# Optimization experiments

Hardware: AMD Instinct MI355X
Metric: run time of the kernel (lower is better)

The kernel has to match this reference:

```python
import jax, jax.numpy as jnp
import numpy as np

B, T, C, H, W = 8, 10, 1, 64, 64
HID = 64

def conv2d_same(x, w):
    return jax.lax.conv_general_dilated(x, w, (1, 1), 'SAME', dimension_numbers=('NCHW', 'OIHW', 'NCHW'))

def setup_inputs():
    key = jax.random.key(0)
    ks = iter(jax.random.split(key, 32))
    inp = {'x': jax.random.uniform(next(ks), (B, T, C, H, W), jnp.float32)}
    def cell_params(prefix, in_ch):
        # 4 gates (i, f, g, o) stacked along output channels -> fused gate conv
        inp[prefix + '_Wx'] = jax.random.normal(next(ks), (4 * HID, in_ch, 3, 3), jnp.float32) * 0.05
        inp[prefix + '_Wh'] = jax.random.normal(next(ks), (4 * HID, HID, 3, 3), jnp.float32) * 0.05
        inp[prefix + '_Wc'] = jax.random.normal(next(ks), (4, HID, H, W), jnp.float32) * 0.05
        inp[prefix + '_b'] = jax.random.normal(next(ks), (4, HID, H, W), jnp.float32) * 0.05
    cell_params('enc0', C)
    cell_params('enc1', HID)
    cell_params('dec0', HID)
    cell_params('dec1', HID)
    inp['fin_w'] = jax.random.normal(next(ks), (1, HID, 3, 3), jnp.float32) * 0.05
    inp['fin_b'] = jnp.zeros((1,), jnp.float32)
    inp['prediction_len'] = 10
    return inp

def _cell(Wx, Wh, Wc, b, xt, h, c):
    # gate = act(W_x*x + W_h*h + W_c.c + bias); all 4 gates use the OLD (h, c)
    hid = h.shape[1]
    pre = conv2d_same(xt, Wx) + conv2d_same(h, Wh)  # (B, 4*hid, H, W)
    pre = pre.reshape(pre.shape[0], 4, hid, pre.shape[2], pre.shape[3])
    pre = pre + Wc[None] * c[:, None] + b[None]
    i = jax.nn.sigmoid(pre[:, 0])
    f = jax.nn.sigmoid(pre[:, 1])
    g = jnp.tanh(pre[:, 2])
    o = jax.nn.sigmoid(pre[:, 3])
    c_new = f * c + i * g
    h_new = o * jnp.tanh(c_new)
    return h_new, c_new

def reference(x, enc0_Wx, enc0_Wh, enc0_Wc, enc0_b, enc1_Wx, enc1_Wh, enc1_Wc, enc1_b, dec0_Wx, dec0_Wh, dec0_Wc, dec0_b, dec1_Wx, dec1_Wh, dec1_Wc, dec1_b, fin_w, fin_b, prediction_len):
    b_, t_ = x.shape[0], x.shape[1]
    h_, w_ = x.shape[3], x.shape[4]
    hid = enc0_Wc.shape[1]
    z = jnp.zeros((b_, hid, h_, w_), x.dtype)

    def enc_step(carry, xt):
        h0, c0, h1, c1 = carry
        h0, c0 = _cell(enc0_Wx, enc0_Wh, enc0_Wc, enc0_b, xt, h0, c0)
        h1, c1 = _cell(enc1_Wx, enc1_Wh, enc1_Wc, enc1_b, h0, h1, c1)
        return (h0, c0, h1, c1), None

    (eh0, ec0, eh1, ec1), _ = jax.lax.scan(enc_step, (z, z, z, z), jnp.swapaxes(x, 0, 1))
    state = eh1  # top-layer encoder hidden; decoder h/c start at zeros (as in torch code)

    def dec_step(carry, _):
        s, h0, c0, h1, c1 = carry
        h0, c0 = _cell(dec0_Wx, dec0_Wh, dec0_Wc, dec0_b, s, h0, c0)
        h1, c1 = _cell(dec1_Wx, dec1_Wh, dec1_Wc, dec1_b, h0, h1, c1)
        return (h1, h0, c0, h1, c1), h1

    _, ys = jax.lax.scan(dec_step, (state, z, z, z, z), None, length=prediction_len)
    # ys: (F, B, hid, H, W); Conv3d with (1,3,3) kernel == per-frame 2d conv
    f_ = ys.shape[0]
    y = ys.reshape(f_ * b_, hid, h_, w_)
    y = conv2d_same(y, fin_w) + fin_b[None, :, None, None]
    y = y.reshape(f_, b_, 1, h_, w_)
    return jax.nn.sigmoid(jnp.swapaxes(y, 0, 1))  # (B, F, 1, H, W)
```

## Files before the change

### kernel.cpp

```cpp
#include <hip/hip_runtime.h>
#include <hip/hip_bf16.h>
#include <math.h>

#define BSZ    8
#define TSTEPS 10
#define FLEN   10
#define HID    64
#define HW     4096
#define IMG    (HID * HW)
#define OC4    (4 * HID)
#define PADW   66
#define PPIX   (PADW * PADW)
#define PADIMG (PPIX * HID)
#define PADSZ  (BSZ * PADIMG)
#define SB     (BSZ * IMG)
#define KT_E0  640
#define KT_STD 1152

typedef __attribute__((ext_vector_type(8))) short bf16x8;
typedef __attribute__((ext_vector_type(4))) float f32x4;

__device__ __forceinline__ float sigmoidf_(float x) {
    return 1.0f / (1.0f + __expf(-x));
}
__device__ __forceinline__ float tanh_fast(float x) {
    float e = __expf(2.0f * x);
    return 1.0f - 2.0f / (e + 1.0f);
}
__device__ __forceinline__ float bf2f(short u) {
    union { unsigned u; float f; } cv;
    cv.u = ((unsigned)(unsigned short)u) << 16;
    return cv.f;
}
__device__ __forceinline__ short f2bf(float x) {
    __hip_bfloat16 h = __float2bfloat16(x);
    union { __hip_bfloat16 h; short s; } cv; cv.h = h;
    return cv.s;
}

__global__ __launch_bounds__(256) void reorder_w(
    const float* __restrict__ Wx, int icx,
    const float* __restrict__ Wh, __hip_bfloat16* __restrict__ Bw, int ktot) {
    int ocp = blockIdx.x, hid = ocp >> 2, gate = ocp & 3;
    int oc = gate * 64 + hid;
    for (int k = threadIdx.x; k < ktot; k += 256) {
        int c = k >> 6, j = k & 63;
        float v;
        if (icx == 1) {
            if (c == 0) v = (j < 9) ? Wx[oc * 9 + j] : 0.0f;
            else        v = Wh[(oc * 64 + j) * 9 + (c - 1)];
        } else {
            if (c < 9)  v = Wx[(oc * 64 + j) * 9 + c];
            else        v = Wh[(oc * 64 + j) * 9 + (c - 9)];
        }
        Bw[ocp * ktot + k] = __float2bfloat16(v);
    }
}

__global__ __launch_bounds__(256) void pack_wcb(
    const float* __restrict__ Wc, const float* __restrict__ bias,
    __hip_bfloat16* __restrict__ wcb) {
    int i = blockIdx.x * 256 + threadIdx.x;
    int hid = i >> 12, p = i & 4095;
    union { short s[8]; bf16x8 v; } u;
#pragma unroll
    for (int g = 0; g < 4; g++) {
        u.s[g]     = f2bf(Wc[(g * HID + hid) * HW + p]);
        u.s[4 + g] = f2bf(bias[(g * HID + hid) * HW + p]);
    }
    *(bf16x8*)&wcb[(size_t)i * 8] = u.v;
}

__global__ __launch_bounds__(256) void pack_x_all(
    const float* __restrict__ x, __hip_bfloat16* __restrict__ px_all) {
    int i = blockIdx.x * 256 + threadIdx.x;
    if (i >= TSTEPS * BSZ * PPIX) return;
    int t = i / (BSZ * PPIX);
    int rem = i - t * (BSZ * PPIX);
    int b = rem / PPIX;
    int pp = rem - b * PPIX;
    int y = pp / PADW, xx = pp - y * PADW;
    int oy = y - 1, ox = xx - 1;
    const float* xb = x + ((size_t)(b * TSTEPS + t)) * HW;
    bool interior = (oy >= 0 && oy < 64 && ox >= 0 && ox < 64);
    union { short s[16]; bf16x8 v[2]; } u;
#pragma unroll
    for (int tap = 0; tap < 9; tap++) {
        int yy = oy + tap / 3 - 1, xc = ox + tap % 3 - 1;
        float val = (interior && yy >= 0 && yy < 64 && xc >= 0 && xc < 64)
                        ? xb[yy * 64 + xc] : 0.0f;
        u.s[tap] = f2bf(val);
    }
#pragma unroll
    for (int tap = 9; tap < 16; tap++) u.s[tap] = 0;
    short* o = (short*)(px_all + (size_t)t * PADSZ + ((size_t)(b * PPIX + pp)) * HID);
    *(bf16x8*)&o[0] = u.v[0];
    *(bf16x8*)&o[8] = u.v[1];
}

struct CellArgs {
    const __hip_bfloat16* Bw;
    const __hip_bfloat16* src0;
    const __hip_bfloat16* src1;
    const __hip_bfloat16* wcb;
    float* cbuf;
    __hip_bfloat16* hout;
    int ktot;
    int n0;
    int first;
};

__global__ __launch_bounds__(256) void gemm_cell_fused(CellArgs A0, CellArgs A1) {
    __shared__ short As[128 * 64];
    __shared__ short Bs[128 * 64];
    const bool z1 = (blockIdx.z != 0);
    const __hip_bfloat16* __restrict__ Bw   = z1 ? A1.Bw   : A0.Bw;
    const __hip_bfloat16* __restrict__ src0 = z1 ? A1.src0 : A0.src0;
    const __hip_bfloat16* __restrict__ src1 = z1 ? A1.src1 : A0.src1;
    const __hip_bfloat16* __restrict__ wcb  = z1 ? A1.wcb  : A0.wcb;
    float* __restrict__ cbuf                = z1 ? A1.cbuf : A0.cbuf;
    __hip_bfloat16* __restrict__ hout       = z1 ? A1.hout : A0.hout;
    const int ktot  = z1 ? A1.ktot  : A0.ktot;
    const int n0    = z1 ? A1.n0    : A0.n0;
    const int first = z1 ? A1.first : A0.first;

    const int tid  = threadIdx.x;
    const int lane = tid & 63;
    const int wave = tid >> 6;
    const int quad = lane >> 4;
    const int l15  = lane & 15;
    const int wr = wave >> 1;
    const int wc = wave & 1;
    const int px0 = blockIdx.x * 128;
    const int oc0 = blockIdx.y * 128;

    int a_off[4], s_off[4];
#pragma unroll
    for (int it = 0; it < 4; it++) {
        int idx = it * 256 + tid;
        int rr = idx >> 3, seg = idx & 7;
        int segx = seg ^ (rr & 7);
        a_off[it] = (oc0 + rr) * ktot + segx * 8;
        int px = px0 + rr;
        int b = px >> 12, p = px & 4095, y = p >> 6, x = p & 63;
        s_off[it] = ((b * PADW + y + 1) * PADW + (x + 1)) * HID + segx * 8;
    }
    const int ldsbase = (tid & ~63) * 8;
    const int xa = l15 & 7;

    f32x4 acc[4][4] = {};
    const int nchunks = n0 + 9;

    for (int kk = 0; kk < nchunks; kk++) {
        const __hip_bfloat16* src;
        int tap;
        if (kk < n0) { src = src0; tap = (n0 == 1) ? 4 : kk; }
        else         { src = src1; tap = kk - n0; }
        int dd = ((tap / 3) - 1) * (PADW * HID) + ((tap % 3) - 1) * HID;
        int ka = kk * 64;
#pragma unroll
        for (int it = 0; it < 4; it++) {
            __builtin_amdgcn_global_load_lds(
                (const __attribute__((address_space(1))) void*)(Bw + a_off[it] + ka),
                (__attribute__((address_space(3))) void*)(&As[it * 2048 + ldsbase]),
                16, 0, 0);
            __builtin_amdgcn_global_load_lds(
                (const __attribute__((address_space(1))) void*)(src + s_off[it] + dd),
                (__attribute__((address_space(3))) void*)(&Bs[it * 2048 + ldsbase]),
                16, 0, 0);
        }
        __syncthreads();
#pragma unroll
        for (int k2 = 0; k2 < 2; k2++) {
            int sA = ((k2 * 4 + quad) ^ xa) * 8;
            bf16x8 af[4], bfr[4];
#pragma unroll
            for (int i = 0; i < 4; i++)
                af[i] = *(const bf16x8*)&As[(wr * 64 + i * 16 + l15) * 64 + sA];
#pragma unroll
            for (int j = 0; j < 4; j++)
                bfr[j] = *(const bf16x8*)&Bs[(wc * 64 + j * 16 + l15) * 64 + sA];
#pragma unroll
            for (int i = 0; i < 4; i++)
#pragma unroll
                for (int j = 0; j < 4; j++)
                    acc[i][j] = __builtin_amdgcn_mfma_f32_16x16x32_bf16(
                        af[i], bfr[j], acc[i][j], 0, 0, 0);
        }
        __syncthreads();
    }

    short* hl = As;
    const int hid0 = oc0 >> 2;
#pragma unroll
    for (int i = 0; i < 4; i++) {
        int hidl = wr * 16 + i * 4 + quad;
        int hid = hid0 + hidl;
#pragma unroll
        for (int j = 0; j < 4; j++) {
            int pxl = wc * 64 + j * 16 + l15;
            int px = px0 + pxl;
            int b = px >> 12, p = px & 4095;
            size_t ci = ((size_t)(b * HID + hid)) * HW + p;
            float cv = first ? 0.0f : cbuf[ci];
            bf16x8 wv = *(const bf16x8*)&wcb[((size_t)hid * HW + p) * 8];
            float pg[4];
#pragma unroll
            for (int r = 0; r < 4; r++)
                pg[r] = acc[i][j][r] + bf2f(wv[r]) * cv + bf2f(wv[4 + r]);
            float ig = sigmoidf_(pg[0]);
            float fg = sigmoidf_(pg[1]);
            float gg = tanh_fast(pg[2]);
            float og = sigmoidf_(pg[3]);
            float cn = fg * cv + ig * gg;
            cbuf[ci] = cn;
            float hn = og * tanh_fast(cn);
            hl[pxl * 40 + hidl] = f2bf(hn);
        }
    }
    __syncthreads();
#pragma unroll
    for (int rnd = 0; rnd < 2; rnd++) {
        int task = rnd * 256 + tid;
        int pxl = task >> 2, q = task & 3;
        bf16x8 v = *(const bf16x8*)&hl[pxl * 40 + q * 8];
        int px = px0 + pxl;
        int b = px >> 12, p = px & 4095, y = p >> 6, x = p & 63;
        *(bf16x8*)&hout[((size_t)((b * PADW + y + 1) * PADW + (x + 1))) * HID
                        + hid0 + q * 8] = v;
    }
}

__global__ __launch_bounds__(256) void final_conv(
    const __hip_bfloat16* __restrict__ ph, const float* __restrict__ fw,
    const float* __restrict__ fb, float* __restrict__ out, int f) {
    int b = blockIdx.y;
    int p = blockIdx.x * 256 + threadIdx.x;
    int y = p >> 6, x = p & 63;
    float acc = fb[0];
#pragma unroll
    for (int tap = 0; tap < 9; tap++) {
        const bf16x8* base = (const bf16x8*)(
            ph + ((b * PADW + y + (tap / 3)) * PADW + (x + (tap % 3))) * HID);
#pragma unroll
        for (int c8 = 0; c8 < 8; c8++) {
            bf16x8 v = base[c8];
#pragma unroll
            for (int jj = 0; jj < 8; jj++)
                acc = fmaf(bf2f(v[jj]), fw[(c8 * 8 + jj) * 9 + tap], acc);
        }
    }
    out[((size_t)(b * FLEN + f)) * HW + p] = sigmoidf_(acc);
}

extern "C" void kernel_launch(void* const* d_in, const int* in_sizes, int n_in,
                              void* d_out, int out_size, void* d_ws, size_t ws_size,
                              hipStream_t stream) {
    const float* x = (const float*)d_in[0];
    const float* Wx_[4] = {(const float*)d_in[1], (const float*)d_in[5],
                           (const float*)d_in[9], (const float*)d_in[13]};
    const float* Wh_[4] = {(const float*)d_in[2], (const float*)d_in[6],
                           (const float*)d_in[10], (const float*)d_in[14]};
    const float* Wc_[4] = {(const float*)d_in[3], (const float*)d_in[7],
                           (const float*)d_in[11], (const float*)d_in[15]};
    const float* b_[4]  = {(const float*)d_in[4], (const float*)d_in[8],
                           (const float*)d_in[12], (const float*)d_in[16]};
    const float* fin_w  = (const float*)d_in[17];
    const float* fin_b  = (const float*)d_in[18];
    float* out = (float*)d_out;

    char* wsb = (char*)d_ws;
    const size_t H_BYTES  = 8ull * PADSZ * sizeof(short);
    const size_t PX_BYTES = 10ull * PADSZ * sizeof(short);
    const size_t C_BYTES  = 4ull * SB * sizeof(float);
    const size_t WCB_ELEM = (size_t)HID * HW * 8;

    __hip_bfloat16* hb = (__hip_bfloat16*)wsb;
    __hip_bfloat16* px_all = (__hip_bfloat16*)(wsb + H_BYTES);
    float* cbuf = (float*)(wsb + H_BYTES + PX_BYTES);
    __hip_bfloat16* wcb = (__hip_bfloat16*)(wsb + H_BYTES + PX_BYTES + C_BYTES);
    __hip_bfloat16* bw = wcb + 4 * WCB_ELEM;

    __hip_bfloat16* e0buf[2] = {hb + 0 * (size_t)PADSZ, hb + 1 * (size_t)PADSZ};
    __hip_bfloat16* e1buf[2] = {hb + 2 * (size_t)PADSZ, hb + 3 * (size_t)PADSZ};
    __hip_bfloat16* d0buf[2] = {hb + 4 * (size_t)PADSZ, hb + 5 * (size_t)PADSZ};
    __hip_bfloat16* d1buf[2] = {hb + 6 * (size_t)PADSZ, hb + 7 * (size_t)PADSZ};

    float* ec0 = cbuf + 0 * (size_t)SB;
    float* ec1 = cbuf + 1 * (size_t)SB;
    float* dc0 = cbuf + 2 * (size_t)SB;
    float* dc1 = cbuf + 3 * (size_t)SB;

    __hip_bfloat16* wcb_[4] = {wcb, wcb + WCB_ELEM, wcb + 2 * WCB_ELEM, wcb + 3 * WCB_ELEM};
    __hip_bfloat16* bw_e0 = bw;
    __hip_bfloat16* bw_e1 = bw_e0 + (size_t)OC4 * KT_E0;
    __hip_bfloat16* bw_d0 = bw_e1 + (size_t)OC4 * KT_STD;
    __hip_bfloat16* bw_d1 = bw_d0 + (size_t)OC4 * KT_STD;
    __hip_bfloat16* bw_[4] = {bw_e0, bw_e1, bw_d0, bw_d1};
    float* c_[4] = {ec0, ec1, dc0, dc1};

    hipMemsetAsync(wsb, 0, H_BYTES, stream);

    reorder_w<<<dim3(OC4), 256, 0, stream>>>(Wx_[0], 1,   Wh_[0], bw_e0, KT_E0);
    reorder_w<<<dim3(OC4), 256, 0, stream>>>(Wx_[1], HID, Wh_[1], bw_e1, KT_STD);
    reorder_w<<<dim3(OC4), 256, 0, stream>>>(Wx_[2], HID, Wh_[2], bw_d0, KT_STD);
    reorder_w<<<dim3(OC4), 256, 0, stream>>>(Wx_[3], HID, Wh_[3], bw_d1, KT_STD);
    for (int cix = 0; cix < 4; cix++)
        pack_wcb<<<dim3((HID * HW) / 256), 256, 0, stream>>>(Wc_[cix], b_[cix], wcb_[cix]);
    pack_x_all<<<dim3((TSTEPS * BSZ * PPIX + 255) / 256), 256, 0, stream>>>(x, px_all);

    auto cellargs = [&](int cell, const __hip_bfloat16* s0, const __hip_bfloat16* s1,
                        __hip_bfloat16* ho, int kt, int nn0, int fi) {
        CellArgs a;
        a.Bw = bw_[cell]; a.src0 = s0; a.src1 = s1; a.wcb = wcb_[cell];
        a.cbuf = c_[cell]; a.hout = ho; a.ktot = kt; a.n0 = nn0; a.first = fi;
        return a;
    };
    auto px = [&](int t) { return px_all + (size_t)t * PADSZ; };

    dim3 gfin(16, BSZ);

    {
        CellArgs a = cellargs(0, px(0), e0buf[1], e0buf[0], KT_E0, 1, 1);
        gemm_cell_fused<<<dim3(256, 2, 1), 256, 0, stream>>>(a, a);
    }
    for (int k = 1; k <= 9; k++) {
        int t0 = k, t1 = k - 1;
        CellArgs a0 = cellargs(0, px(t0), e0buf[(t0 - 1) & 1], e0buf[t0 & 1],
                               KT_E0, 1, 0);
        CellArgs a1 = cellargs(1, e0buf[t1 & 1], e1buf[(t1 - 1) & 1], e1buf[t1 & 1],
                               KT_STD, 9, (t1 == 0) ? 1 : 0);
        gemm_cell_fused<<<dim3(256, 2, 2), 256, 0, stream>>>(a0, a1);
    }
    {
        CellArgs a = cellargs(1, e0buf[1], e1buf[0], e1buf[1], KT_STD, 9, 0);
        gemm_cell_fused<<<dim3(256, 2, 1), 256, 0, stream>>>(a, a);
    }
    __hip_bfloat16* enc_top = e1buf[1];

    for (int f = 0; f < FLEN; f++) {
        const __hip_bfloat16* s = (f == 0) ? enc_top : d1buf[(f - 1) & 1];
        CellArgs a0 = cellargs(2, s, d0buf[(f - 1) & 1], d0buf[f & 1],
                               KT_STD, 9, (f == 0) ? 1 : 0);
        gemm_cell_fused<<<dim3(256, 2, 1), 256, 0, stream>>>(a0, a0);
        CellArgs a1 = cellargs(3, d0buf[f & 1], d1buf[(f - 1) & 1], d1buf[f & 1],
                               KT_STD, 9, (f == 0) ? 1 : 0);
        gemm_cell_fused<<<dim3(256, 2, 1), 256, 0, stream>>>(a1, a1);
        final_conv<<<gfin, 256, 0, stream>>>(d1buf[f & 1], fin_w, fin_b, out, f);
    }
}
```

Measured before the change: 1.567 ms.

## Stage halo tile in LDS for conv GEMM and fuse final conv into decoder launch

The implicit-GEMM cell kernel now loads a padded 4-row by 66-column halo tile of the hidden input into LDS once per source. All 9 taps are read from that tile instead of reloading a shifted 128x64 tile per tap. Weight fragments are read straight from global memory (cache) instead of being staged in LDS. The final output conv for the previous frame runs on extra blocks (blockIdx.y==2) inside the next decoder-0 launch, which removes a separate launch per frame. Risks: uncached weight reads from global memory, bank conflicts on the swizzled halo reads, and larger LDS per block reducing occupancy.

```diff
diff --git a/kernel.cpp b/kernel.cpp
--- a/kernel.cpp
+++ b/kernel.cpp
@@ -110,16 +110,43 @@
     int first;
 };
 
-__global__ __launch_bounds__(256) void gemm_cell_fused(CellArgs A0, CellArgs A1) {
-    __shared__ short As[128 * 64];
-    __shared__ short Bs[128 * 64];
+__global__ __launch_bounds__(256) void gemm_cell_fused(
+    CellArgs A0, CellArgs A1,
+    const __hip_bfloat16* fph, const float* fw, const float* fb,
+    float* fout, int ff) {
+    __shared__ short Hs[264 * 64];
+
+    if (blockIdx.y == 2) {
+        int tid = threadIdx.x;
+        if (tid < 128) {
+            int p = blockIdx.x * 128 + tid;
+            int b = p >> 12, pp = p & 4095;
+            int y = pp >> 6, x = pp & 63;
+            float acc = fb[0];
+#pragma unroll
+            for (int tap = 0; tap < 9; tap++) {
+                const bf16x8* base = (const bf16x8*)(
+                    fph + ((size_t)(b * PADW + y + (tap / 3)) * PADW + (x + (tap % 3))) * HID);
+#pragma unroll
+                for (int c8 = 0; c8 < 8; c8++) {
+                    bf16x8 v = base[c8];
+#pragma unroll
+                    for (int jj = 0; jj < 8; jj++)
+                        acc = fmaf(bf2f(v[jj]), fw[(c8 * 8 + jj) * 9 + tap], acc);
+                }
+            }
+            fout[((size_t)(b * FLEN + ff)) * HW + pp] = sigmoidf_(acc);
+        }
+        return;
+    }
+
     const bool z1 = (blockIdx.z != 0);
-    const __hip_bfloat16* __restrict__ Bw   = z1 ? A1.Bw   : A0.Bw;
     const __hip_bfloat16* __restrict__ src0 = z1 ? A1.src0 : A0.src0;
     const __hip_bfloat16* __restrict__ src1 = z1 ? A1.src1 : A0.src1;
     const __hip_bfloat16* __restrict__ wcb  = z1 ? A1.wcb  : A0.wcb;
     float* __restrict__ cbuf                = z1 ? A1.cbuf : A0.cbuf;
     __hip_bfloat16* __restrict__ hout       = z1 ? A1.hout : A0.hout;
+    const short* __restrict__ BwS = (const short*)(z1 ? A1.Bw : A0.Bw);
     const int ktot  = z1 ? A1.ktot  : A0.ktot;
     const int n0    = z1 ? A1.n0    : A0.n0;
     const int first = z1 ? A1.first : A0.first;
@@ -133,64 +160,87 @@
     const int wc = wave & 1;
     const int px0 = blockIdx.x * 128;
     const int oc0 = blockIdx.y * 128;
-
-    int a_off[4], s_off[4];
-#pragma unroll
-    for (int it = 0; it < 4; it++) {
-        int idx = it * 256 + tid;
-        int rr = idx >> 3, seg = idx & 7;
-        int segx = seg ^ (rr & 7);
-        a_off[it] = (oc0 + rr) * ktot + segx * 8;
-        int px = px0 + rr;
-        int b = px >> 12, p = px & 4095, y = p >> 6, x = p & 63;
-        s_off[it] = ((b * PADW + y + 1) * PADW + (x + 1)) * HID + segx * 8;
-    }
-    const int ldsbase = (tid & ~63) * 8;
-    const int xa = l15 & 7;
+    const int bb = px0 >> 12;
+    const int y0 = (px0 & 4095) >> 6;
+
+    const int abase = (oc0 + wr * 64 + l15) * ktot;
 
     f32x4 acc[4][4] = {};
-    const int nchunks = n0 + 9;
-
-    for (int kk = 0; kk < nchunks; kk++) {
-        const __hip_bfloat16* src;
-        int tap;
-        if (kk < n0) { src = src0; tap = (n0 == 1) ? 4 : kk; }
-        else         { src = src1; tap = kk - n0; }
-        int dd = ((tap / 3) - 1) * (PADW * HID) + ((tap % 3) - 1) * HID;
-        int ka = kk * 64;
-#pragma unroll
-        for (int it = 0; it < 4; it++) {
-            __builtin_amdgcn_global_load_lds(
-                (const __attribute__((address_space(1))) void*)(Bw + a_off[it] + ka),
-                (__attribute__((address_space(3))) void*)(&As[it * 2048 + ldsbase]),
-                16, 0, 0);
-            __builtin_amdgcn_global_load_lds(
-                (const __attribute__((address_space(1))) void*)(src + s_off[it] + dd),
-                (__attribute__((address_space(3))) void*)(&Bs[it * 2048 + ldsbase]),
-                16, 0, 0);
+
+#pragma unroll
+    for (int ph = 0; ph < 2; ph++) {
+        const __hip_bfloat16* src = ph ? src1 : src0;
+        const int cbase = ph ? n0 : 0;
+        const short* sb = (const short*)src +
+                          ((size_t)bb * PPIX + (size_t)y0 * PADW) * HID;
+        if (ph) __syncthreads();
+#pragma unroll
+        for (int r = 0; r < 9; r++) {
+            int idx = r * 256 + tid;
+            if (idx < 2112) {
+                int hp = idx >> 3, seg = idx & 7;
+                int segx = seg ^ (hp & 7);
+                __builtin_amdgcn_global_load_lds(
+                    (const __attribute__((address_space(1))) void*)(sb + hp * 64 + segx * 8),
+                    (__attribute__((address_space(3))) void*)(&Hs[idx * 8]),
+                    16, 0, 0);
+            }
         }
         __syncthreads();
-#pragma unroll
-        for (int k2 = 0; k2 < 2; k2++) {
-            int sA = ((k2 * 4 + quad) ^ xa) * 8;
-            bf16x8 af[4], bfr[4];
-#pragma unroll
-            for (int i = 0; i < 4; i++)
-                af[i] = *(const bf16x8*)&As[(wr * 64 + i * 16 + l15) * 64 + sA];
-#pragma unroll
-            for (int j = 0; j < 4; j++)
-                bfr[j] = *(const bf16x8*)&Bs[(wc * 64 + j * 16 + l15) * 64 + sA];
-#pragma unroll
-            for (int i = 0; i < 4; i++)
-#pragma unroll
-                for (int j = 0; j < 4; j++)
-                    acc[i][j] = __builtin_amdgcn_mfma_f32_16x16x32_bf16(
-                        af[i], bfr[j], acc[i][j], 0, 0, 0);
-        }
-        __syncthreads();
-    }
-
-    short* hl = As;
+
+        if (n0 == 1 && ph == 0) {
+            const int chunk = 0;
+#pragma unroll
+            for (int k2 = 0; k2 < 2; k2++) {
+                bf16x8 af[4], bfr[4];
+#pragma unroll
+                for (int i = 0; i < 4; i++)
+                    af[i] = *(const bf16x8*)(BwS + abase + i * 16 * ktot +
+                                             chunk * 64 + k2 * 32 + quad * 8);
+#pragma unroll
+                for (int j = 0; j < 4; j++) {
+                    int pxl = wc * 64 + j * 16 + l15;
+                    int hp = ((pxl >> 6) + 1) * PADW + (pxl & 63) + 1;
+                    bfr[j] = *(const bf16x8*)&Hs[hp * 64 + (((k2 * 4 + quad) ^ (hp & 7))) * 8];
+                }
+#pragma unroll
+                for (int i = 0; i < 4; i++)
+#pragma unroll
+                    for (int j = 0; j < 4; j++)
+                        acc[i][j] = __builtin_amdgcn_mfma_f32_16x16x32_bf16(
+                            af[i], bfr[j], acc[i][j], 0, 0, 0);
+            }
+        } else {
+#pragma unroll
+            for (int tap = 0; tap < 9; tap++) {
+                const int dy = tap / 3, dx = tap % 3;
+                const int chunk = cbase + tap;
+#pragma unroll
+                for (int k2 = 0; k2 < 2; k2++) {
+                    bf16x8 af[4], bfr[4];
+#pragma unroll
+                    for (int i = 0; i < 4; i++)
+                        af[i] = *(const bf16x8*)(BwS + abase + i * 16 * ktot +
+                                                 chunk * 64 + k2 * 32 + quad * 8);
+#pragma unroll
+                    for (int j = 0; j < 4; j++) {
+                        int pxl = wc * 64 + j * 16 + l15;
+                        int hp = ((pxl >> 6) + dy) * PADW + (pxl & 63) + dx;
+                        bfr[j] = *(const bf16x8*)&Hs[hp * 64 + (((k2 * 4 + quad) ^ (hp & 7))) * 8];
+                    }
+#pragma unroll
+                    for (int i = 0; i < 4; i++)
+#pragma unroll
+                        for (int j = 0; j < 4; j++)
+                            acc[i][j] = __builtin_amdgcn_mfma_f32_16x16x32_bf16(
+                                af[i], bfr[j], acc[i][j], 0, 0, 0);
+                }
+            }
+        }
+    }
+
+    __syncthreads();
+    short* hl = Hs;
     const int hid0 = oc0 >> 2;
 #pragma unroll
     for (int i = 0; i < 4; i++) {
@@ -286,18 +336,13 @@
     __hip_bfloat16* d0buf[2] = {hb + 4 * (size_t)PADSZ, hb + 5 * (size_t)PADSZ};
     __hip_bfloat16* d1buf[2] = {hb + 6 * (size_t)PADSZ, hb + 7 * (size_t)PADSZ};
 
-    float* ec0 = cbuf + 0 * (size_t)SB;
-    float* ec1 = cbuf + 1 * (size_t)SB;
-    float* dc0 = cbuf + 2 * (size_t)SB;
-    float* dc1 = cbuf + 3 * (size_t)SB;
-
+    float* c_[4] = {cbuf, cbuf + (size_t)SB, cbuf + 2 * (size_t)SB, cbuf + 3 * (size_t)SB};
     __hip_bfloat16* wcb_[4] = {wcb, wcb + WCB_ELEM, wcb + 2 * WCB_ELEM, wcb + 3 * WCB_ELEM};
     __hip_bfloat16* bw_e0 = bw;
     __hip_bfloat16* bw_e1 = bw_e0 + (size_t)OC4 * KT_E0;
     __hip_bfloat16* bw_d0 = bw_e1 + (size_t)OC4 * KT_STD;
     __hip_bfloat16* bw_d1 = bw_d0 + (size_t)OC4 * KT_STD;
     __hip_bfloat16* bw_[4] = {bw_e0, bw_e1, bw_d0, bw_d1};
-    float* c_[4] = {ec0, ec1, dc0, dc1};
 
     hipMemsetAsync(wsb, 0, H_BYTES, stream);
 
@@ -318,11 +363,10 @@
     };
     auto px = [&](int t) { return px_all + (size_t)t * PADSZ; };
 
-    dim3 gfin(16, BSZ);
-
     {
         CellArgs a = cellargs(0, px(0), e0buf[1], e0buf[0], KT_E0, 1, 1);
-        gemm_cell_fused<<<dim3(256, 2, 1), 256, 0, stream>>>(a, a);
+        gemm_cell_fused<<<dim3(256, 2, 1), 256, 0, stream>>>(
+            a, a, (const __hip_bfloat16*)nullptr, fin_w, fin_b, out, 0);
     }
     for (int k = 1; k <= 9; k++) {
         int t0 = k, t1 = k - 1;
@@ -330,11 +374,13 @@
                                KT_E0, 1, 0);
         CellArgs a1 = cellargs(1, e0buf[t1 & 1], e1buf[(t1 - 1) & 1], e1buf[t1 & 1],
                                KT_STD, 9, (t1 == 0) ? 1 : 0);
-        gemm_cell_fused<<<dim3(256, 2, 2), 256, 0, stream>>>(a0, a1);
+        gemm_cell_fused<<<dim3(256, 2, 2), 256, 0, stream>>>(
+            a0, a1, (const __hip_bfloat16*)nullptr, fin_w, fin_b, out, 0);
     }
     {
         CellArgs a = cellargs(1, e0buf[1], e1buf[0], e1buf[1], KT_STD, 9, 0);
-        gemm_cell_fused<<<dim3(256, 2, 1), 256, 0, stream>>>(a, a);
+        gemm_cell_fused<<<dim3(256, 2, 1), 256, 0, stream>>>(
+            a, a, (const __hip_bfloat16*)nullptr, fin_w, fin_b, out, 0);
     }
     __hip_bfloat16* enc_top = e1buf[1];
 
@@ -342,10 +388,17 @@
         const __hip_bfloat16* s = (f == 0) ? enc_top : d1buf[(f - 1) & 1];
         CellArgs a0 = cellargs(2, s, d0buf[(f - 1) & 1], d0buf[f & 1],
                                KT_STD, 9, (f == 0) ? 1 : 0);
-        gemm_cell_fused<<<dim3(256, 2, 1), 256, 0, stream>>>(a0, a0);
+        if (f == 0) {
+            gemm_cell_fused<<<dim3(256, 2, 1), 256, 0, stream>>>(
+                a0, a0, (const __hip_bfloat16*)nullptr, fin_w, fin_b, out, 0);
+        } else {
+            gemm_cell_fused<<<dim3(256, 3, 1), 256, 0, stream>>>(
+                a0, a0, d1buf[(f - 1) & 1], fin_w, fin_b, out, f - 1);
+        }
         CellArgs a1 = cellargs(3, d0buf[f & 1], d1buf[(f - 1) & 1], d1buf[f & 1],
                                KT_STD, 9, (f == 0) ? 1 : 0);
-        gemm_cell_fused<<<dim3(256, 2, 1), 256, 0, stream>>>(a1, a1);
-        final_conv<<<gfin, 256, 0, stream>>>(d1buf[f & 1], fin_w, fin_b, out, f);
-    }
-}
+        gemm_cell_fused<<<dim3(256, 2, 1), 256, 0, stream>>>(
+            a1, a1, (const __hip_bfloat16*)nullptr, fin_w, fin_b, out, 0);
+    }
+    final_conv<<<dim3(16, BSZ), 256, 0, stream>>>(d1buf[1], fin_w, fin_b, out, 9);
+}
```

Result: slower. 2.835 ms (+81.0%).
